# Optimization experiments

Measured on AMD Instinct MI355X. Metric: run time of the kernel, lower is better.

The kernel has to match this reference:

```python
import jax, jax.numpy as jnp
import numpy as np

NEG = -100.0  # pad value used by the original skew trick


def setup_inputs() -> dict:
    key = jax.random.key(0)
    kq, ke = jax.random.split(key)
    b, h, L, d = 2, 8, 2048, 64
    q = jax.random.normal(kq, (b, h, L, d), dtype=jnp.float32)
    e = jax.random.normal(ke, (h, L, d), dtype=jnp.float32)  # learned rel-pos embeddings
    return {"q": q, "e": e}


def reference(q, e):
    # mode == 'fix': seq_len_src == seq_len_tgt == L
    b, h, L, d = q.shape
    bh = b * h
    # QE^T: (b,h,L,d) x (h,L,d) -> (b,h,L,L); e is shared across batch
    rel = jnp.einsum('bhld,hmd->bhlm', q, e)
    rel = rel.reshape(bh, L, L)
    # skew: prepend a -100 column, reshape (bh, L+1, L), drop first row
    rel = jnp.pad(rel, ((0, 0), (0, 0), (1, 0)), constant_values=NEG)
    rel = rel.reshape(bh, L + 1, L)[:, 1:, :][:, :L, :]
    # zero out strictly-upper triangle (masked_fill with triu(diag=1))
    mask = jnp.triu(jnp.ones((L, L), dtype=bool), k=1)
    rel = jnp.where(mask[None, :, :], jnp.float32(0.0), rel)
    return rel.reshape(b, h, L, L)
```

## Files before the change

kernel.cpp:

```cpp
#include <hip/hip_runtime.h>
#include <hip/hip_bf16.h>


typedef __bf16 bf16x8 __attribute__((ext_vector_type(8)));
typedef float  f32x4  __attribute__((ext_vector_type(4)));
typedef float  f32x8  __attribute__((ext_vector_type(8)));

constexpr int L     = 2048;
constexpr int D     = 64;
constexpr int LDW   = 100;
constexpr int EROWS = 192;

__device__ __forceinline__ bf16x8 load_cvt8(const float* __restrict__ p) {
  f32x8 v = *(const f32x8*)p;
  bf16x8 r;
#pragma unroll
  for (int k = 0; k < 8; ++k) r[k] = (__bf16)v[k];
  return r;
}

__global__ __launch_bounds__(512) void skew_band(const float* __restrict__ q,
                                                 const float* __restrict__ e,
                                                 float* __restrict__ out) {
  const int tid  = threadIdx.x;
  const int lane = tid & 63;
  const int w    = tid >> 6;
  const int ln   = lane & 15;
  const int quad = lane >> 4;
  const int i    = blockIdx.x;
  const int h    = i & 7;
  const int p    = blockIdx.y;
  const int seg  = blockIdx.z;

  __shared__ ushort elds[2 * EROWS * 64];
  __shared__ __align__(16) float stg[8 * 16 * LDW];

  {
    const int rcol = tid & 7;
#pragma unroll
    for (int g = 0; g < 2; ++g) {
      const int Kg    = g ? (15 - p) : p;
      const int nbase = (Kg << 7) - 64;
#pragma unroll
      for (int pass = 0; pass < 3; ++pass) {
        const int row = (tid >> 3) + (pass << 6);
        const int n   = nbase + row;
        if (n >= 0) {
          const int erow = 2047 - n;
          bf16x8 v = load_cvt8(e + ((size_t)(h * L + erow)) * D + rcol * 8);
          *(bf16x8*)&elds[g * (EROWS * 64) + row * 64 +
                          ((rcol * 8) ^ ((row & 7) << 3))] = v;
        }
      }
    }
  }
  __syncthreads();

  float* obase = out + (size_t)i * L * L;
  float* ldsw  = &stg[w * (16 * LDW)];

#pragma unroll 1
  for (int t = 0; t < 32; ++t) {
    const int u   = w + (seg << 3) + (t << 4);
    const int s0i = u & 127;
    const int sel = u >> 7;
    const int g   = sel & 1;
    const int a   = sel >> 1;
    const int s0  = s0i << 4;
    const int Kg  = g ? (15 - p) : p;

    const int cb = (s0 >> 6) - 2 * Kg - a;
    if (cb >= 0) {
      const int c0   = cb << 6;
      const int M    = s0 - c0;
      const int tmin = (M >= 64) ? 0 : ((64 - M) >> 4);
      const bool mask = (M < 64);
      const int rowb = (s0 & 63) + (a << 6);
      const int gbase = g * (EROWS * 64);

      const float* qp = q + ((size_t)(i * L + s0 + ln)) * D + (quad << 3);
      const bf16x8 a0 = load_cvt8(qp);
      const bf16x8 a1 = load_cvt8(qp + 32);

      f32x4 acc[5];
#pragma unroll
      for (int tt = 0; tt < 5; ++tt) {
        if (tt < tmin) continue;
        const int row = rowb + (tt << 4) + ln;
        const int rb  = gbase + row * 64;
        const int sw  = (row & 7) << 3;
        const bf16x8 b0 = *(const bf16x8*)&elds[rb + (((quad << 3)     ) ^ sw)];
        const bf16x8 b1 = *(const bf16x8*)&elds[rb + ((32 + (quad << 3)) ^ sw)];
        f32x4 z = {0.f, 0.f, 0.f, 0.f};
        z       = __builtin_amdgcn_mfma_f32_16x16x32_bf16(a0, b0, z, 0, 0, 0);
        acc[tt] = __builtin_amdgcn_mfma_f32_16x16x32_bf16(a1, b1, z, 0, 0, 0);
      }

      const int lbase = quad * (4 * LDW - 4) + ln + 15;
#pragma unroll
      for (int tt = 0; tt < 5; ++tt) {
        if (tt < tmin) continue;
#pragma unroll
        for (int jr = 0; jr < 4; ++jr)
          ldsw[lbase + jr * (LDW - 1) + (tt << 4)] = acc[tt][jr];
      }

      float* orow = obase + (size_t)s0 * L + c0;
#pragma unroll
      for (int it = 0; it < 4; ++it) {
        const int idx = (it << 6) + lane;
        const int rr  = idx >> 4;
        const int jj  = idx & 15;
        const f32x4 v = *(const f32x4*)&ldsw[rr * LDW + 76 - (jj << 2)];
        f32x4 o = { v[3], v[2], v[1], v[0] };
        if (mask) {
          const int lim = M + rr - (jj << 2);
#pragma unroll
          for (int t2 = 0; t2 < 4; ++t2) if (t2 > lim) o[t2] = 0.f;
        }
        __builtin_nontemporal_store(
            o, (f32x4*)(orow + (size_t)rr * L + (jj << 2)));
      }
    }

    const int cbz = (s0 >> 6) + 2 * Kg + 1 + a;
    if (cbz <= 31) {
      float* orow = obase + (size_t)s0 * L + (cbz << 6);
      const f32x4 zz = {0.f, 0.f, 0.f, 0.f};
#pragma unroll
      for (int it = 0; it < 4; ++it) {
        const int idx = (it << 6) + lane;
        const int rr  = idx >> 4;
        const int jj  = idx & 15;
        __builtin_nontemporal_store(
            zz, (f32x4*)(orow + (size_t)rr * L + (jj << 2)));
      }
    }
  }
}

extern "C" void kernel_launch(void* const* d_in, const int* in_sizes, int n_in,
                              void* d_out, int out_size, void* d_ws, size_t ws_size,
                              hipStream_t stream) {
  const float* q = (const float*)d_in[0];
  const float* e = (const float*)d_in[1];
  float* out = (float*)d_out;

  dim3 grid(16, 8, 2);
  skew_band<<<grid, 512, 0, stream>>>(q, e, out);
}
```

Measured before the change: 285.8 us.

## Reorder loop to reuse Q fragments, prefetch next Q, use plain stores

The flat 32-iteration loop becomes an outer loop over 8 row strips with an inner loop over the 4 (g,a) band selectors. Each Q fragment is then loaded and converted once per strip instead of four times. The next strip's Q rows are prefetched into registers while the current strip computes, to hide global load latency. Nontemporal stores are swapped for ordinary stores, which changes how the write-dominated output interacts with the cache, and the extra live prefetch registers could affect occupancy.

```diff
diff --git a/kernel.cpp b/kernel.cpp
--- a/kernel.cpp
+++ b/kernel.cpp
@@ -11,12 +11,15 @@
 constexpr int LDW   = 100;
 constexpr int EROWS = 192;
 
-__device__ __forceinline__ bf16x8 load_cvt8(const float* __restrict__ p) {
-  f32x8 v = *(const f32x8*)p;
+__device__ __forceinline__ bf16x8 cvt8(f32x8 v) {
   bf16x8 r;
 #pragma unroll
   for (int k = 0; k < 8; ++k) r[k] = (__bf16)v[k];
   return r;
+}
+
+__device__ __forceinline__ bf16x8 load_cvt8(const float* __restrict__ p) {
+  return cvt8(*(const f32x8*)p);
 }
 
 __global__ __launch_bounds__(512) void skew_band(const float* __restrict__ q,
@@ -59,81 +62,92 @@
   float* obase = out + (size_t)i * L * L;
   float* ldsw  = &stg[w * (16 * LDW)];
 
+  const int s0i0 = w + (seg << 3);
+  const float* qbase = q + ((size_t)(i * L + (s0i0 << 4) + ln)) * D + (quad << 3);
+
+  f32x8 r0 = *(const f32x8*)qbase;
+  f32x8 r1 = *(const f32x8*)(qbase + 32);
+
 #pragma unroll 1
-  for (int t = 0; t < 32; ++t) {
-    const int u   = w + (seg << 3) + (t << 4);
-    const int s0i = u & 127;
-    const int sel = u >> 7;
-    const int g   = sel & 1;
-    const int a   = sel >> 1;
+  for (int k = 0; k < 8; ++k) {
+    const bf16x8 a0 = cvt8(r0);
+    const bf16x8 a1 = cvt8(r1);
+    if (k < 7) {
+      const float* qn = qbase + (size_t)(k + 1) * (256 * D);
+      r0 = *(const f32x8*)qn;
+      r1 = *(const f32x8*)(qn + 32);
+    }
+
+    const int s0i = s0i0 + (k << 4);
     const int s0  = s0i << 4;
-    const int Kg  = g ? (15 - p) : p;
+    const int cbb = s0i >> 2;
 
-    const int cb = (s0 >> 6) - 2 * Kg - a;
-    if (cb >= 0) {
-      const int c0   = cb << 6;
-      const int M    = s0 - c0;
-      const int tmin = (M >= 64) ? 0 : ((64 - M) >> 4);
-      const bool mask = (M < 64);
-      const int rowb = (s0 & 63) + (a << 6);
-      const int gbase = g * (EROWS * 64);
+#pragma unroll 1
+    for (int sel = 0; sel < 4; ++sel) {
+      const int g  = sel & 1;
+      const int a  = sel >> 1;
+      const int Kg = g ? (15 - p) : p;
 
-      const float* qp = q + ((size_t)(i * L + s0 + ln)) * D + (quad << 3);
-      const bf16x8 a0 = load_cvt8(qp);
-      const bf16x8 a1 = load_cvt8(qp + 32);
+      const int cb = cbb - 2 * Kg - a;
+      if (cb >= 0) {
+        const int c0    = cb << 6;
+        const int M     = s0 - c0;
+        const int tmin  = (M >= 64) ? 0 : ((64 - M) >> 4);
+        const bool mask = (M < 64);
+        const int rowb  = (s0 & 63) + (a << 6);
+        const int gbase = g * (EROWS * 64);
 
-      f32x4 acc[5];
+        f32x4 acc[5];
 #pragma unroll
-      for (int tt = 0; tt < 5; ++tt) {
-        if (tt < tmin) continue;
-        const int row = rowb + (tt << 4) + ln;
-        const int rb  = gbase + row * 64;
-        const int sw  = (row & 7) << 3;
-        const bf16x8 b0 = *(const bf16x8*)&elds[rb + (((quad << 3)     ) ^ sw)];
-        const bf16x8 b1 = *(const bf16x8*)&elds[rb + ((32 + (quad << 3)) ^ sw)];
-        f32x4 z = {0.f, 0.f, 0.f, 0.f};
-        z       = __builtin_amdgcn_mfma_f32_16x16x32_bf16(a0, b0, z, 0, 0, 0);
-        acc[tt] = __builtin_amdgcn_mfma_f32_16x16x32_bf16(a1, b1, z, 0, 0, 0);
+        for (int tt = 0; tt < 5; ++tt) {
+          if (tt < tmin) continue;
+          const int row = rowb + (tt << 4) + ln;
+          const int rb  = gbase + row * 64;
+          const int sw  = (row & 7) << 3;
+          const bf16x8 b0 = *(const bf16x8*)&elds[rb + (((quad << 3)     ) ^ sw)];
+          const bf16x8 b1 = *(const bf16x8*)&elds[rb + ((32 + (quad << 3)) ^ sw)];
+          f32x4 z = {0.f, 0.f, 0.f, 0.f};
+          z       = __builtin_amdgcn_mfma_f32_16x16x32_bf16(a0, b0, z, 0, 0, 0);
+          acc[tt] = __builtin_amdgcn_mfma_f32_16x16x32_bf16(a1, b1, z, 0, 0, 0);
+        }
+
+        const int lbase = quad * (4 * LDW - 4) + ln + 15;
+#pragma unroll
+        for (int tt = 0; tt < 5; ++tt) {
+          if (tt < tmin) continue;
+#pragma unroll
+          for (int jr = 0; jr < 4; ++jr)
+            ldsw[lbase + jr * (LDW - 1) + (tt << 4)] = acc[tt][jr];
+        }
+
+        float* orow = obase + (size_t)s0 * L + c0;
+#pragma unroll
+        for (int it = 0; it < 4; ++it) {
+          const int idx = (it << 6) + lane;
+          const int rr  = idx >> 4;
+          const int jj  = idx & 15;
+          const f32x4 v = *(const f32x4*)&ldsw[rr * LDW + 76 - (jj << 2)];
+          f32x4 o = { v[3], v[2], v[1], v[0] };
+          if (mask) {
+            const int lim = M + rr - (jj << 2);
+#pragma unroll
+            for (int t2 = 0; t2 < 4; ++t2) if (t2 > lim) o[t2] = 0.f;
+          }
+          *(f32x4*)(orow + (size_t)rr * L + (jj << 2)) = o;
+        }
       }
 
-      const int lbase = quad * (4 * LDW - 4) + ln + 15;
+      const int cbz = cbb + 2 * Kg + 1 + a;
+      if (cbz <= 31) {
+        float* orow = obase + (size_t)s0 * L + (cbz << 6);
+        const f32x4 zz = {0.f, 0.f, 0.f, 0.f};
 #pragma unroll
-      for (int tt = 0; tt < 5; ++tt) {
-        if (tt < tmin) continue;
-#pragma unroll
-        for (int jr = 0; jr < 4; ++jr)
-          ldsw[lbase + jr * (LDW - 1) + (tt << 4)] = acc[tt][jr];
-      }
-
-      float* orow = obase + (size_t)s0 * L + c0;
-#pragma unroll
-      for (int it = 0; it < 4; ++it) {
-        const int idx = (it << 6) + lane;
-        const int rr  = idx >> 4;
-        const int jj  = idx & 15;
-        const f32x4 v = *(const f32x4*)&ldsw[rr * LDW + 76 - (jj << 2)];
-        f32x4 o = { v[3], v[2], v[1], v[0] };
-        if (mask) {
-          const int lim = M + rr - (jj << 2);
-#pragma unroll
-          for (int t2 = 0; t2 < 4; ++t2) if (t2 > lim) o[t2] = 0.f;
+        for (int it = 0; it < 4; ++it) {
+          const int idx = (it << 6) + lane;
+          const int rr  = idx >> 4;
+          const int jj  = idx & 15;
+          *(f32x4*)(orow + (size_t)rr * L + (jj << 2)) = zz;
         }
-        __builtin_nontemporal_store(
-            o, (f32x4*)(orow + (size_t)rr * L + (jj << 2)));
-      }
-    }
-
-    const int cbz = (s0 >> 6) + 2 * Kg + 1 + a;
-    if (cbz <= 31) {
-      float* orow = obase + (size_t)s0 * L + (cbz << 6);
-      const f32x4 zz = {0.f, 0.f, 0.f, 0.f};
-#pragma unroll
-      for (int it = 0; it < 4; ++it) {
-        const int idx = (it << 6) + lane;
-        const int rr  = idx >> 4;
-        const int jj  = idx & 15;
-        __builtin_nontemporal_store(
-            zz, (f32x4*)(orow + (size_t)rr * L + (jj << 2)));
       }
     }
   }
```

Result: faster. 274.1 us (-4.1%).
